# Performance work log

Measured on AMD Instinct MI355X. Metric: run time of the kernel, lower is better.

## Reference

```python
import jax, jax.numpy as jnp
import numpy as np

N, D_IN, D_H = 8192, 512, 512


def setup_inputs() -> dict:
    key = jax.random.key(0)
    kH, kWq, kbq, kWk, kbk = jax.random.split(key, 5)
    s_in = 1.0 / np.sqrt(D_IN)
    return {
        "H": jax.random.normal(kH, (N, D_IN), dtype=jnp.float32),
        "Wq": jax.random.normal(kWq, (D_IN, D_H), dtype=jnp.float32) * s_in,
        "bq": jax.random.normal(kbq, (D_H,), dtype=jnp.float32) * 0.01,
        "Wk": jax.random.normal(kWk, (D_IN, D_H), dtype=jnp.float32) * s_in,
        "bk": jax.random.normal(kbk, (D_H,), dtype=jnp.float32) * 0.01,
    }


def reference(H, Wq, bq, Wk, bk):
    # H: [N, T]; Q, K: [N, d_h]
    Q = H @ Wq + bq
    K = H @ Wk + bk
    # A: [N, N] raw scores
    A = Q @ K.T
    n = A.shape[0]
    # torch.where(eye, 0, A): zero out the diagonal BEFORE scale/softmax
    A = A.at[jnp.arange(n), jnp.arange(n)].set(0.0)
    A = A / jnp.sqrt(jnp.asarray(K.shape[-1], A.dtype))
    A = jax.nn.softmax(A, axis=-1)
    # aggregate values (= H itself) and add residual
    return A @ H + H
```

## Files before the change

kernel.cpp:

```cpp
#include <hip/hip_runtime.h>
#include <cstdint>
#include <cstddef>

#define GLOBAL_AS __attribute__((address_space(1)))
#define LDS_AS __attribute__((address_space(3)))

typedef __attribute__((ext_vector_type(8))) short short8;
typedef __attribute__((ext_vector_type(4))) float floatx4;
typedef __attribute__((ext_vector_type(2))) long long2v;
typedef __attribute__((ext_vector_type(4))) int int4v;
typedef __attribute__((ext_vector_type(8))) int int8v;

#if defined(__has_builtin)
#if __has_builtin(__builtin_amdgcn_cvt_pk_fp8_f32)
#define HAVE_HW_FP8 1
#endif
#endif

static __device__ __forceinline__ unsigned short f2bf(float f) {
  uint32_t u = __builtin_bit_cast(uint32_t, f);
  u += 0x7fffu + ((u >> 16) & 1u);
  return (unsigned short)(u >> 16);
}

static __device__ __forceinline__ unsigned char f2fp8(float f) {
#ifdef HAVE_HW_FP8
  float c = fminf(fmaxf(f, -448.f), 448.f);
  return (unsigned char)(__builtin_amdgcn_cvt_pk_fp8_f32(c, 0.f, 0, false) & 0xff);
#else
  unsigned char s = 0;
  if (f < 0.f) { s = 0x80; f = -f; }
  if (f >= 448.f) return s | 0x7e;
  if (f < 0.015625f) { int r = (int)(f * 512.f + 0.5f); return s | (unsigned char)r; }
  uint32_t u = __builtin_bit_cast(uint32_t, f);
  int e = (int)((u >> 23) & 0xff) - 127;
  uint32_t keep = (u >> 20) & 7, rest = u & 0xfffffu;
  if (rest > 0x80000u || (rest == 0x80000u && (keep & 1))) ++keep;
  if (keep == 8) { keep = 0; ++e; }
  if (e > 8) return s | 0x7e;
  return s | (unsigned char)(((e + 7) << 3) | keep);
#endif
}

static __device__ __forceinline__ uint32_t pack4fp8(const float e[4]) {
#ifdef HAVE_HW_FP8
  const uint32_t p01 = (uint32_t)__builtin_amdgcn_cvt_pk_fp8_f32(e[0], e[1], 0, false);
  const uint32_t p23 = (uint32_t)__builtin_amdgcn_cvt_pk_fp8_f32(e[2], e[3], 0, false);
  return (p01 & 0xffffu) | (p23 << 16);
#else
  return (uint32_t)f2fp8(e[0]) | ((uint32_t)f2fp8(e[1]) << 8) |
         ((uint32_t)f2fp8(e[2]) << 16) | ((uint32_t)f2fp8(e[3]) << 24);
#endif
}


static __device__ __forceinline__ void wait_vm0() {
  __builtin_amdgcn_s_waitcnt(0x0f70);
}

static __device__ __forceinline__ int8v load_frag32(const unsigned char* base, int row, int quad) {
  const int h = row & 7;
  const int c0 = (2 * quad) ^ h;
  const int c1 = (2 * quad + 1) ^ h;
  const int4v lo = *(const int4v*)(base + row * 128 + c0 * 16);
  const int4v hi = *(const int4v*)(base + row * 128 + c1 * 16);
  int8v r;
  r[0] = lo[0]; r[1] = lo[1]; r[2] = lo[2]; r[3] = lo[3];
  r[4] = hi[0]; r[5] = hi[1]; r[6] = hi[2]; r[7] = hi[3];
  return r;
}

static __device__ __forceinline__ floatx4 mx_mfma(int8v a, int8v b, floatx4 c) {
  return __builtin_amdgcn_mfma_scale_f32_16x16x128_f8f6f4(a, b, c, 0, 0, 0, 0x7f, 0, 0x7f);
}

__global__ __launch_bounds__(256) void transpose_h_kernel(
    const float* __restrict__ in, unsigned char* __restrict__ outT8,
    unsigned short* __restrict__ outN, float* __restrict__ outF,
    int R, int C) {
  __shared__ float t[64][65];
  const int bc = blockIdx.x * 64;
  const int br = blockIdx.y * 64;
  const int tc = threadIdx.x & 63;
  const int tr = threadIdx.x >> 6;
  for (int r = tr; r < 64; r += 4) {
    const float v = in[(size_t)(br + r) * C + bc + tc];
    t[r][tc] = v;
    outN[(size_t)(br + r) * C + bc + tc] = f2bf(v);
    outF[(size_t)(br + r) * C + bc + tc] = v;
  }
  __syncthreads();
  const int tperm = 4 * (tc & 15) + (tc >> 4);
  for (int r = tr; r < 64; r += 4)
    outT8[(size_t)(bc + r) * R + br + tperm] = f2fp8(t[tc][r]);
}

__global__ __launch_bounds__(256) void transpose_w2_kernel(
    const float* __restrict__ Wq, const float* __restrict__ Wk,
    unsigned short* __restrict__ outT, int Dd) {
  const float* in = blockIdx.z ? Wk : Wq;
  unsigned short* out = outT + (size_t)blockIdx.z * Dd * Dd;
  __shared__ float t[64][65];
  const int bc = blockIdx.x * 64;
  const int br = blockIdx.y * 64;
  const int tc = threadIdx.x & 63;
  const int tr = threadIdx.x >> 6;
  for (int r = tr; r < 64; r += 4)
    t[r][tc] = in[(size_t)(br + r) * Dd + bc + tc];
  __syncthreads();
  for (int r = tr; r < 64; r += 4)
    out[(size_t)(bc + r) * Dd + br + tc] = f2bf(t[tc][r]);
}

__global__ __launch_bounds__(256) void pack_bias_kernel(
    const float* __restrict__ bq, const float* __restrict__ bk,
    float* __restrict__ bqk) {
  int i = blockIdx.x * 256 + threadIdx.x;
  bqk[i] = (i < 512) ? bq[i] : bk[i - 512];
}

__global__ __launch_bounds__(256, 4) void gemm_proj(
    const unsigned short* __restrict__ A,
    const unsigned short* __restrict__ Bt,
    int Ncols, int K,
    const float* __restrict__ bias,
    unsigned char* __restrict__ C8)
{
  __shared__ unsigned short As[2][128 * 32];
  __shared__ unsigned short Bs[2][128 * 32];

  const int tid  = threadIdx.x;
  const int lane = tid & 63;
  const int wave = tid >> 6;
  const int wr   = (wave >> 1) * 64;
  const int wc   = (wave & 1) * 64;
  const int quad = lane >> 4;
  const int l15  = lane & 15;
  const int bm   = blockIdx.y * 128;
  const int bn   = blockIdx.x * 128;

  const int c0 = tid, c1 = tid + 256;
  const int r0a = c0 >> 2, k0a = (((c0 & 3) ^ ((c0 >> 3) & 3)) << 3);
  const int r1a = c1 >> 2, k1a = (((c1 & 3) ^ ((c1 >> 3) & 3)) << 3);

  auto stage = [&](int kt, int b) {
    __builtin_amdgcn_global_load_lds(
        (const GLOBAL_AS void*)(A + (size_t)(bm + r0a) * K + kt + k0a),
        (LDS_AS void*)(&As[b][c0 * 8]), 16, 0, 0);
    __builtin_amdgcn_global_load_lds(
        (const GLOBAL_AS void*)(A + (size_t)(bm + r1a) * K + kt + k1a),
        (LDS_AS void*)(&As[b][c1 * 8]), 16, 0, 0);
    __builtin_amdgcn_global_load_lds(
        (const GLOBAL_AS void*)(Bt + (size_t)(bn + r0a) * K + kt + k0a),
        (LDS_AS void*)(&Bs[b][c0 * 8]), 16, 0, 0);
    __builtin_amdgcn_global_load_lds(
        (const GLOBAL_AS void*)(Bt + (size_t)(bn + r1a) * K + kt + k1a),
        (LDS_AS void*)(&Bs[b][c1 * 8]), 16, 0, 0);
  };

  floatx4 acc[4][4];
#pragma unroll
  for (int i = 0; i < 4; ++i)
#pragma unroll
    for (int j = 0; j < 4; ++j)
      acc[i][j] = (floatx4){0.f, 0.f, 0.f, 0.f};

  stage(0, 0);
  const int swq = quad ^ ((l15 >> 1) & 3);
  const int nIter = K >> 5;
  for (int it = 0; it < nIter; ++it) {
    const int b = it & 1;
    wait_vm0();
    __syncthreads();
    if (it + 1 < nIter) stage((it + 1) << 5, b ^ 1);

    short8 af[4], bfr[4];
#pragma unroll
    for (int i = 0; i < 4; ++i)
      af[i] = *(const short8*)(&As[b][(wr + i * 16 + l15) * 32 + swq * 8]);
#pragma unroll
    for (int j = 0; j < 4; ++j)
      bfr[j] = *(const short8*)(&Bs[b][(wc + j * 16 + l15) * 32 + swq * 8]);
#pragma unroll
    for (int i = 0; i < 4; ++i)
#pragma unroll
      for (int j = 0; j < 4; ++j)
        acc[i][j] = __builtin_amdgcn_mfma_f32_16x16x32_bf16(af[i], bfr[j], acc[i][j], 0, 0, 0);
  }

#pragma unroll
  for (int i = 0; i < 4; ++i) {
    const int rl = bm + wr + i * 16 + quad * 4;
#pragma unroll
    for (int r = 0; r < 4; ++r) {
      const int row = rl + r;
      float e[4];
#pragma unroll
      for (int j = 0; j < 4; ++j)
        e[j] = acc[i][j][r] + bias[bn + wc + j * 16 + l15];
      const uint32_t d = pack4fp8(e);
      *(uint32_t*)(C8 + (size_t)row * Ncols + bn + wc + 4 * l15) = d;
    }
  }
}

__global__ __launch_bounds__(256, 4) void gemm_qk8(
    const unsigned char* __restrict__ A,
    const unsigned char* __restrict__ Bt,
    int Ncols, int K, int lda, int ldb,
    float* __restrict__ lsum,
    int row0,
    unsigned char* __restrict__ P8)
{
  __shared__ unsigned char As[2][128 * 64];
  __shared__ unsigned char Bs[2][128 * 64];

  const int tid  = threadIdx.x;
  const int lane = tid & 63;
  const int wave = tid >> 6;
  const int wr   = (wave >> 1) * 64;
  const int wc   = (wave & 1) * 64;
  const int quad = lane >> 4;
  const int l15  = lane & 15;

  int bxn = blockIdx.x, byn = blockIdx.y;
  if (gridDim.x == 64 && gridDim.y == 64) {
    const int id = blockIdx.y * 64 + blockIdx.x;
    const int r = id & 7, w = id >> 3;
    bxn = (r & 3) * 16 + (w & 15);
    byn = (r >> 2) * 32 + (w >> 4);
  }
  const int bm = byn * 128;
  const int bn = bxn * 128;

  const int c0 = tid, c1 = tid + 256;
  const int r0a = c0 >> 2, k0a = (((c0 & 3) ^ ((c0 >> 3) & 3)) << 4);
  const int r1a = c1 >> 2, k1a = (((c1 & 3) ^ ((c1 >> 3) & 3)) << 4);

  auto stage = [&](int kt, int b) {
    __builtin_amdgcn_global_load_lds(
        (const GLOBAL_AS void*)(A + (size_t)(bm + r0a) * lda + kt + k0a),
        (LDS_AS void*)(&As[b][c0 * 16]), 16, 0, 0);
    __builtin_amdgcn_global_load_lds(
        (const GLOBAL_AS void*)(A + (size_t)(bm + r1a) * lda + kt + k1a),
        (LDS_AS void*)(&As[b][c1 * 16]), 16, 0, 0);
    __builtin_amdgcn_global_load_lds(
        (const GLOBAL_AS void*)(Bt + (size_t)(bn + r0a) * ldb + kt + k0a),
        (LDS_AS void*)(&Bs[b][c0 * 16]), 16, 0, 0);
    __builtin_amdgcn_global_load_lds(
        (const GLOBAL_AS void*)(Bt + (size_t)(bn + r1a) * ldb + kt + k1a),
        (LDS_AS void*)(&Bs[b][c1 * 16]), 16, 0, 0);
  };

  floatx4 acc[4][4];
#pragma unroll
  for (int i = 0; i < 4; ++i)
#pragma unroll
    for (int j = 0; j < 4; ++j)
      acc[i][j] = (floatx4){0.f, 0.f, 0.f, 0.f};

  stage(0, 0);
  const int swq = quad ^ ((l15 >> 1) & 3);
  const int nIter = K >> 6;
  for (int it = 0; it < nIter; ++it) {
    const int b = it & 1;
    wait_vm0();
    __syncthreads();
    if (it + 1 < nIter) stage((it + 1) << 6, b ^ 1);

    long2v af[4], bfr[4];
#pragma unroll
    for (int i = 0; i < 4; ++i)
      af[i] = *(const long2v*)(&As[b][(wr + i * 16 + l15) * 64 + swq * 16]);
#pragma unroll
    for (int j = 0; j < 4; ++j)
      bfr[j] = *(const long2v*)(&Bs[b][(wc + j * 16 + l15) * 64 + swq * 16]);
#pragma unroll
    for (int i = 0; i < 4; ++i)
#pragma unroll
      for (int j = 0; j < 4; ++j) {
        acc[i][j] = __builtin_amdgcn_mfma_f32_16x16x32_fp8_fp8(af[i].x, bfr[j].x, acc[i][j], 0, 0, 0);
        acc[i][j] = __builtin_amdgcn_mfma_f32_16x16x32_fp8_fp8(af[i].y, bfr[j].y, acc[i][j], 0, 0, 0);
      }
  }

  const float scale = 0.044194173824159216f;
#pragma unroll
  for (int i = 0; i < 4; ++i) {
    const int rl = bm + wr + i * 16 + quad * 4;
#pragma unroll
    for (int r = 0; r < 4; ++r) {
      const int row = rl + r;
      float e4[4];
#pragma unroll
      for (int j = 0; j < 4; ++j) {
        const int col = bn + wc + j * 16 + l15;
        const float lg = ((row0 + row) == col) ? 0.f : acc[i][j][r] * scale;
        e4[j] = fminf(__expf(lg), 448.f);
      }
      float rsum = (e4[0] + e4[1]) + (e4[2] + e4[3]);
      const uint32_t d = pack4fp8(e4);
      *(uint32_t*)(P8 + (size_t)row * Ncols + bn + wc + 4 * l15) = d;
      rsum += __shfl_xor(rsum, 1);
      rsum += __shfl_xor(rsum, 2);
      rsum += __shfl_xor(rsum, 4);
      rsum += __shfl_xor(rsum, 8);
      if (l15 == 0) atomicAdd(&lsum[row0 + row], rsum);
    }
  }
}

__global__ __launch_bounds__(256, 3) void gemm_pv8(
    const unsigned char* __restrict__ P,
    const unsigned char* __restrict__ Bt,
    int Kchunk,
    const float* __restrict__ lvec,
    int row0,
    float* __restrict__ out)
{
  __shared__ unsigned char As[2][64 * 128];
  __shared__ unsigned char Bs[2][128 * 128];

  const int tid  = threadIdx.x;
  const int lane = tid & 63;
  const int wave = tid >> 6;
  const int wr   = (wave >> 1) * 32;
  const int wc   = (wave & 1) * 64;
  const int quad = lane >> 4;
  const int l15  = lane & 15;

  int bxn = blockIdx.x, byn = blockIdx.y;
  if (gridDim.x == 4 && gridDim.y == 128) {
    const int id2 = blockIdx.y * 4 + blockIdx.x;
    const int xcd = id2 & 7, w = id2 >> 3;
    bxn = w & 3;
    byn = xcd * 16 + (w >> 2);
  }
  const int bm = byn * 64;
  const int bn = bxn * 128;
  const int k0 = blockIdx.z * Kchunk;

  const int a0 = tid, a1 = tid + 256;
  const int ar0 = a0 >> 3, ac0 = ((a0 & 7) ^ (ar0 & 7)) << 4;
  const int ar1 = a1 >> 3, ac1 = ((a1 & 7) ^ (ar1 & 7)) << 4;
  const int b0 = tid, b1 = tid + 256, b2 = tid + 512, b3 = tid + 768;
  const int br0 = b0 >> 3, bc0 = ((b0 & 7) ^ (br0 & 7)) << 4;
  const int br1 = b1 >> 3, bc1 = ((b1 & 7) ^ (br1 & 7)) << 4;
  const int br2 = b2 >> 3, bc2 = ((b2 & 7) ^ (br2 & 7)) << 4;
  const int br3 = b3 >> 3, bc3 = ((b3 & 7) ^ (br3 & 7)) << 4;

  auto stage = [&](int kt, int b) {
    __builtin_amdgcn_global_load_lds(
        (const GLOBAL_AS void*)(P + (size_t)(bm + ar0) * 8192 + kt + ac0),
        (LDS_AS void*)(&As[b][a0 * 16]), 16, 0, 0);
    __builtin_amdgcn_global_load_lds(
        (const GLOBAL_AS void*)(P + (size_t)(bm + ar1) * 8192 + kt + ac1),
        (LDS_AS void*)(&As[b][a1 * 16]), 16, 0, 0);
    __builtin_amdgcn_global_load_lds(
        (const GLOBAL_AS void*)(Bt + (size_t)(bn + br0) * 8192 + kt + bc0),
        (LDS_AS void*)(&Bs[b][b0 * 16]), 16, 0, 0);
    __builtin_amdgcn_global_load_lds(
        (const GLOBAL_AS void*)(Bt + (size_t)(bn + br1) * 8192 + kt + bc1),
        (LDS_AS void*)(&Bs[b][b1 * 16]), 16, 0, 0);
    __builtin_amdgcn_global_load_lds(
        (const GLOBAL_AS void*)(Bt + (size_t)(bn + br2) * 8192 + kt + bc2),
        (LDS_AS void*)(&Bs[b][b2 * 16]), 16, 0, 0);
    __builtin_amdgcn_global_load_lds(
        (const GLOBAL_AS void*)(Bt + (size_t)(bn + br3) * 8192 + kt + bc3),
        (LDS_AS void*)(&Bs[b][b3 * 16]), 16, 0, 0);
  };

  floatx4 acc[2][4];
#pragma unroll
  for (int i = 0; i < 2; ++i)
#pragma unroll
    for (int j = 0; j < 4; ++j)
      acc[i][j] = (floatx4){0.f, 0.f, 0.f, 0.f};

  stage(k0, 0);
  const int nIter = Kchunk >> 7;
  for (int it = 0; it < nIter; ++it) {
    const int b = it & 1;
    wait_vm0();
    __syncthreads();
    if (it + 1 < nIter) stage(k0 + ((it + 1) << 7), b ^ 1);

    const int8v af0 = load_frag32(As[b], wr + l15, quad);
    const int8v af1 = load_frag32(As[b], wr + 16 + l15, quad);
#pragma unroll
    for (int j = 0; j < 4; ++j) {
      const int8v bf = load_frag32(Bs[b], wc + j * 16 + l15, quad);
      acc[0][j] = mx_mfma(af0, bf, acc[0][j]);
      acc[1][j] = mx_mfma(af1, bf, acc[1][j]);
    }
  }

#pragma unroll
  for (int i = 0; i < 2; ++i) {
    const int rl = bm + wr + i * 16 + quad * 4;
#pragma unroll
    for (int r = 0; r < 4; ++r) {
      const int grow = row0 + rl + r;
      const float inv = 1.f / lvec[grow];
#pragma unroll
      for (int j = 0; j < 4; ++j) {
        const int col = bn + wc + j * 16 + l15;
        atomicAdd(&out[(size_t)grow * 512 + col], acc[i][j][r] * inv);
      }
    }
  }
}

extern "C" void kernel_launch(void* const* d_in, const int* in_sizes, int n_in,
                              void* d_out, int out_size, void* d_ws, size_t ws_size,
                              hipStream_t stream) {
  const float* H  = (const float*)d_in[0];
  const float* Wq = (const float*)d_in[1];
  const float* bq = (const float*)d_in[2];
  const float* Wk = (const float*)d_in[3];
  const float* bk = (const float*)d_in[4];
  float* out = (float*)d_out;

  const int N = 8192, D = 512;

  char* ws = (char*)d_ws;
  size_t off = 0;
  auto alloc = [&](size_t bytes) { char* p = ws + off; off += bytes; return p; };
  unsigned short* Hb   = (unsigned short*)alloc((size_t)N * D * 2);
  unsigned char*  HbT8 = (unsigned char*)alloc((size_t)D * N);
  unsigned char*  QK8  = (unsigned char*)alloc((size_t)N * 2 * D);
  unsigned short* BqkT = (unsigned short*)alloc((size_t)2 * D * D * 2);
  float* bqk = (float*)alloc((size_t)2 * D * 4);
  float* l   = (float*)alloc((size_t)N * 4);
  const size_t base = off;
  unsigned char* P8 = (unsigned char*)(ws + base);

  const size_t pBytes = (size_t)N * N;
  const size_t avail = (ws_size > base) ? (ws_size - base) : 0;
  const bool fullP = (avail >= pBytes);

  hipMemsetAsync(l, 0, (size_t)N * 4, stream);
  transpose_h_kernel<<<dim3(D / 64, N / 64), 256, 0, stream>>>(H, HbT8, Hb, out, N, D);
  transpose_w2_kernel<<<dim3(D / 64, D / 64, 2), 256, 0, stream>>>(Wq, Wk, BqkT, D);
  pack_bias_kernel<<<dim3(4), 256, 0, stream>>>(bq, bk, bqk);

  gemm_proj<<<dim3(2 * D / 128, N / 128), 256, 0, stream>>>(
      Hb, BqkT, 2 * D, D, bqk, QK8);

  if (fullP) {
    gemm_qk8<<<dim3(N / 128, N / 128), 256, 0, stream>>>(
        QK8, QK8 + D, N, D, 2 * D, 2 * D, l, 0, P8);
    gemm_pv8<<<dim3(D / 128, N / 64, 2), 256, 0, stream>>>(
        P8, HbT8, N / 2, l, 0, out);
  } else {
    int maxRows = (int)(avail / (size_t)N);
    maxRows &= ~127;
    if (maxRows < 128) maxRows = 128;
    for (int r0 = 0; r0 < N; r0 += maxRows) {
      int rows = N - r0;
      if (rows > maxRows) rows = maxRows;
      gemm_qk8<<<dim3(N / 128, rows / 128), 256, 0, stream>>>(
          QK8 + (size_t)r0 * 2 * D, QK8 + D, N, D, 2 * D, 2 * D, l, r0, P8);
      gemm_pv8<<<dim3(D / 128, rows / 64, 1), 256, 0, stream>>>(
          P8, HbT8, N, l, r0, out);
    }
  }
}
```

Baseline: 261.6 us.

## Enlarge QK GEMM tile to 256x256 with triple-buffered, phased LDS pipeline

Rewrites the QK^T FP8 GEMM to use 512-thread blocks computing 256x256 tiles instead of 256-thread 128x128 tiles. It triple-buffers LDS, issues prefetches two K-steps ahead in halves interleaved with MFMA phases, and separates the phases with barriers and s_setprio. The aim is to raise arithmetic intensity and global-load reuse while hiding load latency. In exchange it uses much more LDS and registers (one block per CU), adds more barriers, and launches only 1024 blocks.

Result: slower. 278.9 us (+6.6%).

```diff
diff --git a/kernel.cpp b/kernel.cpp
--- a/kernel.cpp
+++ b/kernel.cpp
@@ -57,6 +57,17 @@
 static __device__ __forceinline__ void wait_vm0() {
   __builtin_amdgcn_s_waitcnt(0x0f70);
 }
+static __device__ __forceinline__ void wait_vm4() {
+  __builtin_amdgcn_s_waitcnt(0x0f74);
+}
+static __device__ __forceinline__ void sfence() {
+  __builtin_amdgcn_sched_barrier(0);
+}
+static __device__ __forceinline__ void phase_bar() {
+  sfence();
+  __builtin_amdgcn_s_barrier();
+  sfence();
+}
 
 static __device__ __forceinline__ int8v load_frag32(const unsigned char* base, int row, int quad) {
   const int h = row & 7;
@@ -204,7 +215,7 @@
   }
 }
 
-__global__ __launch_bounds__(256, 4) void gemm_qk8(
+__global__ __launch_bounds__(512, 1) void gemm_qk8(
     const unsigned char* __restrict__ A,
     const unsigned char* __restrict__ Bt,
     int Ncols, int K, int lda, int ldb,
@@ -212,95 +223,148 @@
     int row0,
     unsigned char* __restrict__ P8)
 {
-  __shared__ unsigned char As[2][128 * 64];
-  __shared__ unsigned char Bs[2][128 * 64];
+  __shared__ unsigned char AsB[3][256 * 64];
+  __shared__ unsigned char BsB[3][256 * 64];
 
   const int tid  = threadIdx.x;
   const int lane = tid & 63;
   const int wave = tid >> 6;
-  const int wr   = (wave >> 1) * 64;
-  const int wc   = (wave & 1) * 64;
+  const int wm   = wave >> 2;
+  const int wn   = wave & 3;
   const int quad = lane >> 4;
   const int l15  = lane & 15;
 
   int bxn = blockIdx.x, byn = blockIdx.y;
-  if (gridDim.x == 64 && gridDim.y == 64) {
-    const int id = blockIdx.y * 64 + blockIdx.x;
+  if (gridDim.x == 32 && gridDim.y == 32) {
+    const int id = blockIdx.y * 32 + blockIdx.x;
     const int r = id & 7, w = id >> 3;
-    bxn = (r & 3) * 16 + (w & 15);
-    byn = (r >> 2) * 32 + (w >> 4);
-  }
-  const int bm = byn * 128;
-  const int bn = bxn * 128;
-
-  const int c0 = tid, c1 = tid + 256;
-  const int r0a = c0 >> 2, k0a = (((c0 & 3) ^ ((c0 >> 3) & 3)) << 4);
-  const int r1a = c1 >> 2, k1a = (((c1 & 3) ^ ((c1 >> 3) & 3)) << 4);
-
-  auto stage = [&](int kt, int b) {
-    __builtin_amdgcn_global_load_lds(
-        (const GLOBAL_AS void*)(A + (size_t)(bm + r0a) * lda + kt + k0a),
-        (LDS_AS void*)(&As[b][c0 * 16]), 16, 0, 0);
-    __builtin_amdgcn_global_load_lds(
-        (const GLOBAL_AS void*)(A + (size_t)(bm + r1a) * lda + kt + k1a),
-        (LDS_AS void*)(&As[b][c1 * 16]), 16, 0, 0);
-    __builtin_amdgcn_global_load_lds(
-        (const GLOBAL_AS void*)(Bt + (size_t)(bn + r0a) * ldb + kt + k0a),
-        (LDS_AS void*)(&Bs[b][c0 * 16]), 16, 0, 0);
-    __builtin_amdgcn_global_load_lds(
-        (const GLOBAL_AS void*)(Bt + (size_t)(bn + r1a) * ldb + kt + k1a),
-        (LDS_AS void*)(&Bs[b][c1 * 16]), 16, 0, 0);
+    bxn = (r & 3) * 8 + (w & 7);
+    byn = (r >> 2) * 16 + (w >> 3);
+  }
+  const int bm = byn * 256;
+  const int bn = bxn * 256;
+
+  const int srow128 = tid >> 2;
+  const int schunk  = tid & 3;
+  auto stage_h = [&](int kt, unsigned char* la, unsigned char* lb, int h) {
+    const int row  = h * 128 + srow128;
+    const int gcol = ((schunk ^ ((row >> 1) & 3)) << 4);
+    __builtin_amdgcn_global_load_lds(
+        (const GLOBAL_AS void*)(A + (size_t)(bm + row) * lda + kt + gcol),
+        (LDS_AS void*)(la + row * 64 + schunk * 16), 16, 0, 0);
+    __builtin_amdgcn_global_load_lds(
+        (const GLOBAL_AS void*)(Bt + (size_t)(bn + row) * ldb + kt + gcol),
+        (LDS_AS void*)(lb + row * 64 + schunk * 16), 16, 0, 0);
   };
 
-  floatx4 acc[4][4];
-#pragma unroll
-  for (int i = 0; i < 4; ++i)
+  floatx4 acc[8][4];
+#pragma unroll
+  for (int i = 0; i < 8; ++i)
 #pragma unroll
     for (int j = 0; j < 4; ++j)
       acc[i][j] = (floatx4){0.f, 0.f, 0.f, 0.f};
 
-  stage(0, 0);
+  unsigned char *a0 = AsB[0], *a1 = AsB[1], *a2 = AsB[2];
+  unsigned char *b0 = BsB[0], *b1 = BsB[1], *b2 = BsB[2];
+
+  stage_h(0, a0, b0, 0);  stage_h(0, a0, b0, 1);
+  stage_h(64, a1, b1, 0); stage_h(64, a1, b1, 1);
+
   const int swq = quad ^ ((l15 >> 1) & 3);
-  const int nIter = K >> 6;
-  for (int it = 0; it < nIter; ++it) {
-    const int b = it & 1;
-    wait_vm0();
-    __syncthreads();
-    if (it + 1 < nIter) stage((it + 1) << 6, b ^ 1);
-
-    long2v af[4], bfr[4];
-#pragma unroll
-    for (int i = 0; i < 4; ++i)
-      af[i] = *(const long2v*)(&As[b][(wr + i * 16 + l15) * 64 + swq * 16]);
-#pragma unroll
-    for (int j = 0; j < 4; ++j)
-      bfr[j] = *(const long2v*)(&Bs[b][(wc + j * 16 + l15) * 64 + swq * 16]);
-#pragma unroll
-    for (int i = 0; i < 4; ++i)
-#pragma unroll
-      for (int j = 0; j < 4; ++j) {
-        acc[i][j] = __builtin_amdgcn_mfma_f32_16x16x32_fp8_fp8(af[i].x, bfr[j].x, acc[i][j], 0, 0, 0);
-        acc[i][j] = __builtin_amdgcn_mfma_f32_16x16x32_fp8_fp8(af[i].y, bfr[j].y, acc[i][j], 0, 0, 0);
+  const int nT = K >> 6;
+
+  long2v aF[4], bF0[2], bF1[2];
+
+  for (int t = 0; t < nT; ++t) {
+    if (t + 1 < nT) wait_vm4(); else wait_vm0();
+    phase_bar();
+
+    const unsigned char* ca = a0;
+    const unsigned char* cb = b0;
+    const bool pf  = (t + 2 < nT);
+    const int  kt2 = (t + 2) << 6;
+
+#pragma unroll
+    for (int ii = 0; ii < 4; ++ii)
+      aF[ii] = *(const long2v*)(ca + (wm * 128 + ii * 16 + l15) * 64 + swq * 16);
+#pragma unroll
+    for (int jj = 0; jj < 2; ++jj)
+      bF0[jj] = *(const long2v*)(cb + (wn * 64 + jj * 16 + l15) * 64 + swq * 16);
+    if (pf) stage_h(kt2, a2, b2, 0);
+    phase_bar();
+    __builtin_amdgcn_s_setprio(1);
+#pragma unroll
+    for (int ii = 0; ii < 4; ++ii)
+#pragma unroll
+      for (int jj = 0; jj < 2; ++jj) {
+        acc[ii][jj] = __builtin_amdgcn_mfma_f32_16x16x32_fp8_fp8(aF[ii].x, bF0[jj].x, acc[ii][jj], 0, 0, 0);
+        acc[ii][jj] = __builtin_amdgcn_mfma_f32_16x16x32_fp8_fp8(aF[ii].y, bF0[jj].y, acc[ii][jj], 0, 0, 0);
       }
+    __builtin_amdgcn_s_setprio(0);
+    phase_bar();
+
+#pragma unroll
+    for (int jj = 0; jj < 2; ++jj)
+      bF1[jj] = *(const long2v*)(cb + (wn * 64 + 32 + jj * 16 + l15) * 64 + swq * 16);
+    if (pf) stage_h(kt2, a2, b2, 1);
+    phase_bar();
+    __builtin_amdgcn_s_setprio(1);
+#pragma unroll
+    for (int ii = 0; ii < 4; ++ii)
+#pragma unroll
+      for (int jj = 0; jj < 2; ++jj) {
+        acc[ii][2 + jj] = __builtin_amdgcn_mfma_f32_16x16x32_fp8_fp8(aF[ii].x, bF1[jj].x, acc[ii][2 + jj], 0, 0, 0);
+        acc[ii][2 + jj] = __builtin_amdgcn_mfma_f32_16x16x32_fp8_fp8(aF[ii].y, bF1[jj].y, acc[ii][2 + jj], 0, 0, 0);
+      }
+    __builtin_amdgcn_s_setprio(0);
+    phase_bar();
+
+#pragma unroll
+    for (int ii = 0; ii < 4; ++ii)
+      aF[ii] = *(const long2v*)(ca + (wm * 128 + 64 + ii * 16 + l15) * 64 + swq * 16);
+    phase_bar();
+    __builtin_amdgcn_s_setprio(1);
+#pragma unroll
+    for (int ii = 0; ii < 4; ++ii)
+#pragma unroll
+      for (int jj = 0; jj < 2; ++jj) {
+        acc[4 + ii][2 + jj] = __builtin_amdgcn_mfma_f32_16x16x32_fp8_fp8(aF[ii].x, bF1[jj].x, acc[4 + ii][2 + jj], 0, 0, 0);
+        acc[4 + ii][2 + jj] = __builtin_amdgcn_mfma_f32_16x16x32_fp8_fp8(aF[ii].y, bF1[jj].y, acc[4 + ii][2 + jj], 0, 0, 0);
+      }
+    __builtin_amdgcn_s_setprio(0);
+    phase_bar();
+
+    __builtin_amdgcn_s_setprio(1);
+#pragma unroll
+    for (int ii = 0; ii < 4; ++ii)
+#pragma unroll
+      for (int jj = 0; jj < 2; ++jj) {
+        acc[4 + ii][jj] = __builtin_amdgcn_mfma_f32_16x16x32_fp8_fp8(aF[ii].x, bF0[jj].x, acc[4 + ii][jj], 0, 0, 0);
+        acc[4 + ii][jj] = __builtin_amdgcn_mfma_f32_16x16x32_fp8_fp8(aF[ii].y, bF0[jj].y, acc[4 + ii][jj], 0, 0, 0);
+      }
+    __builtin_amdgcn_s_setprio(0);
+
+    unsigned char* ta = a0; a0 = a1; a1 = a2; a2 = ta;
+    unsigned char* tb = b0; b0 = b1; b1 = b2; b2 = tb;
   }
 
   const float scale = 0.044194173824159216f;
 #pragma unroll
-  for (int i = 0; i < 4; ++i) {
-    const int rl = bm + wr + i * 16 + quad * 4;
+  for (int i = 0; i < 8; ++i) {
+    const int rl = bm + wm * 128 + i * 16 + quad * 4;
 #pragma unroll
     for (int r = 0; r < 4; ++r) {
       const int row = rl + r;
       float e4[4];
 #pragma unroll
       for (int j = 0; j < 4; ++j) {
-        const int col = bn + wc + j * 16 + l15;
+        const int col = bn + wn * 64 + j * 16 + l15;
         const float lg = ((row0 + row) == col) ? 0.f : acc[i][j][r] * scale;
         e4[j] = fminf(__expf(lg), 448.f);
       }
       float rsum = (e4[0] + e4[1]) + (e4[2] + e4[3]);
       const uint32_t d = pack4fp8(e4);
-      *(uint32_t*)(P8 + (size_t)row * Ncols + bn + wc + 4 * l15) = d;
+      *(uint32_t*)(P8 + (size_t)row * Ncols + bn + wn * 64 + 4 * l15) = d;
       rsum += __shfl_xor(rsum, 1);
       rsum += __shfl_xor(rsum, 2);
       rsum += __shfl_xor(rsum, 4);
@@ -448,18 +512,18 @@
       Hb, BqkT, 2 * D, D, bqk, QK8);
 
   if (fullP) {
-    gemm_qk8<<<dim3(N / 128, N / 128), 256, 0, stream>>>(
+    gemm_qk8<<<dim3(N / 256, N / 256), 512, 0, stream>>>(
         QK8, QK8 + D, N, D, 2 * D, 2 * D, l, 0, P8);
     gemm_pv8<<<dim3(D / 128, N / 64, 2), 256, 0, stream>>>(
         P8, HbT8, N / 2, l, 0, out);
   } else {
     int maxRows = (int)(avail / (size_t)N);
-    maxRows &= ~127;
-    if (maxRows < 128) maxRows = 128;
+    maxRows &= ~255;
+    if (maxRows < 256) maxRows = 256;
     for (int r0 = 0; r0 < N; r0 += maxRows) {
       int rows = N - r0;
       if (rows > maxRows) rows = maxRows;
-      gemm_qk8<<<dim3(N / 128, rows / 128), 256, 0, stream>>>(
+      gemm_qk8<<<dim3(N / 256, rows / 256), 512, 0, stream>>>(
           QK8 + (size_t)r0 * 2 * D, QK8 + D, N, D, 2 * D, 2 * D, l, r0, P8);
       gemm_pv8<<<dim3(D / 128, rows / 64, 1), 256, 0, stream>>>(
           P8, HbT8, N, l, r0, out);
```

## Load P fragments directly to registers in PV GEMM, staging only B in LDS

Applied to the files above, without the earlier changes.

The PV GEMM no longer stages the P (A operand) tile through shared memory. Each wave now loads its own A fragments straight from global memory into registers, double-buffered with two register sets, while only Bt keeps going through LDS with global_load_lds. The loop is unrolled by two so the register buffers alternate. This removes LDS traffic and LDS space for A, but the direct per-lane global loads are less coalesced and hold more registers; the wait_vm0 before each barrier still waits on these loads.

After: 277.2 us. 1.06x slower.

```diff
diff --git a/kernel.cpp b/kernel.cpp
--- a/kernel.cpp
+++ b/kernel.cpp
@@ -70,6 +70,13 @@
   return r;
 }
 
+static __device__ __forceinline__ int8v cat8(int4v lo, int4v hi) {
+  int8v r;
+  r[0] = lo[0]; r[1] = lo[1]; r[2] = lo[2]; r[3] = lo[3];
+  r[4] = hi[0]; r[5] = hi[1]; r[6] = hi[2]; r[7] = hi[3];
+  return r;
+}
+
 static __device__ __forceinline__ floatx4 mx_mfma(int8v a, int8v b, floatx4 c) {
   return __builtin_amdgcn_mfma_scale_f32_16x16x128_f8f6f4(a, b, c, 0, 0, 0, 0x7f, 0, 0x7f);
 }
@@ -318,7 +325,6 @@
     int row0,
     float* __restrict__ out)
 {
-  __shared__ unsigned char As[2][64 * 128];
   __shared__ unsigned char Bs[2][128 * 128];
 
   const int tid  = threadIdx.x;
@@ -340,22 +346,13 @@
   const int bn = bxn * 128;
   const int k0 = blockIdx.z * Kchunk;
 
-  const int a0 = tid, a1 = tid + 256;
-  const int ar0 = a0 >> 3, ac0 = ((a0 & 7) ^ (ar0 & 7)) << 4;
-  const int ar1 = a1 >> 3, ac1 = ((a1 & 7) ^ (ar1 & 7)) << 4;
   const int b0 = tid, b1 = tid + 256, b2 = tid + 512, b3 = tid + 768;
   const int br0 = b0 >> 3, bc0 = ((b0 & 7) ^ (br0 & 7)) << 4;
   const int br1 = b1 >> 3, bc1 = ((b1 & 7) ^ (br1 & 7)) << 4;
   const int br2 = b2 >> 3, bc2 = ((b2 & 7) ^ (br2 & 7)) << 4;
   const int br3 = b3 >> 3, bc3 = ((b3 & 7) ^ (br3 & 7)) << 4;
 
-  auto stage = [&](int kt, int b) {
-    __builtin_amdgcn_global_load_lds(
-        (const GLOBAL_AS void*)(P + (size_t)(bm + ar0) * 8192 + kt + ac0),
-        (LDS_AS void*)(&As[b][a0 * 16]), 16, 0, 0);
-    __builtin_amdgcn_global_load_lds(
-        (const GLOBAL_AS void*)(P + (size_t)(bm + ar1) * 8192 + kt + ac1),
-        (LDS_AS void*)(&As[b][a1 * 16]), 16, 0, 0);
+  auto stageB = [&](int kt, int b) {
     __builtin_amdgcn_global_load_lds(
         (const GLOBAL_AS void*)(Bt + (size_t)(bn + br0) * 8192 + kt + bc0),
         (LDS_AS void*)(&Bs[b][b0 * 16]), 16, 0, 0);
@@ -370,6 +367,9 @@
         (LDS_AS void*)(&Bs[b][b3 * 16]), 16, 0, 0);
   };
 
+  const unsigned char* ap0 = P + (size_t)(bm + wr + l15) * 8192 + quad * 32;
+  const unsigned char* ap1 = P + (size_t)(bm + wr + 16 + l15) * 8192 + quad * 32;
+
   floatx4 acc[2][4];
 #pragma unroll
   for (int i = 0; i < 2; ++i)
@@ -377,21 +377,56 @@
     for (int j = 0; j < 4; ++j)
       acc[i][j] = (floatx4){0.f, 0.f, 0.f, 0.f};
 
-  stage(k0, 0);
+  int4v xa0lo, xa0hi, xa1lo, xa1hi;
+  int4v ya0lo, ya0hi, ya1lo, ya1hi;
+
+  stageB(k0, 0);
+  xa0lo = *(const int4v*)(ap0 + k0);
+  xa0hi = *(const int4v*)(ap0 + k0 + 16);
+  xa1lo = *(const int4v*)(ap1 + k0);
+  xa1hi = *(const int4v*)(ap1 + k0 + 16);
+
   const int nIter = Kchunk >> 7;
-  for (int it = 0; it < nIter; ++it) {
-    const int b = it & 1;
-    wait_vm0();
-    __syncthreads();
-    if (it + 1 < nIter) stage(k0 + ((it + 1) << 7), b ^ 1);
-
-    const int8v af0 = load_frag32(As[b], wr + l15, quad);
-    const int8v af1 = load_frag32(As[b], wr + 16 + l15, quad);
-#pragma unroll
-    for (int j = 0; j < 4; ++j) {
-      const int8v bf = load_frag32(Bs[b], wc + j * 16 + l15, quad);
-      acc[0][j] = mx_mfma(af0, bf, acc[0][j]);
-      acc[1][j] = mx_mfma(af1, bf, acc[1][j]);
+  for (int it = 0; it < nIter; it += 2) {
+    {
+      wait_vm0();
+      __syncthreads();
+      const int kn = k0 + ((it + 1) << 7);
+      if (it + 1 < nIter) {
+        stageB(kn, 1);
+        ya0lo = *(const int4v*)(ap0 + kn);
+        ya0hi = *(const int4v*)(ap0 + kn + 16);
+        ya1lo = *(const int4v*)(ap1 + kn);
+        ya1hi = *(const int4v*)(ap1 + kn + 16);
+      }
+      const int8v af0 = cat8(xa0lo, xa0hi);
+      const int8v af1 = cat8(xa1lo, xa1hi);
+#pragma unroll
+      for (int j = 0; j < 4; ++j) {
+        const int8v bf = load_frag32(Bs[0], wc + j * 16 + l15, quad);
+        acc[0][j] = mx_mfma(af0, bf, acc[0][j]);
+        acc[1][j] = mx_mfma(af1, bf, acc[1][j]);
+      }
+    }
+    if (it + 1 < nIter) {
+      wait_vm0();
+      __syncthreads();
+      const int kn = k0 + ((it + 2) << 7);
+      if (it + 2 < nIter) {
+        stageB(kn, 0);
+        xa0lo = *(const int4v*)(ap0 + kn);
+        xa0hi = *(const int4v*)(ap0 + kn + 16);
+        xa1lo = *(const int4v*)(ap1 + kn);
+        xa1hi = *(const int4v*)(ap1 + kn + 16);
+      }
+      const int8v af0 = cat8(ya0lo, ya0hi);
+      const int8v af1 = cat8(ya1lo, ya1hi);
+#pragma unroll
+      for (int j = 0; j < 4; ++j) {
+        const int8v bf = load_frag32(Bs[1], wc + j * 16 + l15, quad);
+        acc[0][j] = mx_mfma(af0, bf, acc[0][j]);
+        acc[1][j] = mx_mfma(af1, bf, acc[1][j]);
+      }
     }
   }
 
```
